# Kernel optimization log

Measured on AMD Instinct MI355X. Metric: run time of the kernel, lower is better.

Reference implementation:

```python
import jax, jax.numpy as jnp
import numpy as np

B, C, H, W = 8, 256, 128, 128
BN_EPS = 1e-5

def setup_inputs() -> dict:
    key = jax.random.key(0)
    ks = jax.random.split(key, 7)
    scale = 1.0 / np.sqrt(C)
    x = jax.random.normal(ks[0], (B, C, H, W), dtype=jnp.float32)
    w_qkv = jax.random.normal(ks[1], (3 * C, C), dtype=jnp.float32) * scale
    w_proj = jax.random.normal(ks[2], (C, C), dtype=jnp.float32) * scale
    gamma = jax.random.uniform(ks[3], (C,), dtype=jnp.float32)
    beta = jax.random.normal(ks[4], (C,), dtype=jnp.float32)
    running_mean = jax.random.normal(ks[5], (C,), dtype=jnp.float32)
    running_var = jax.random.uniform(ks[6], (C,), dtype=jnp.float32) + 0.5
    return {"x": x, "w_qkv": w_qkv, "w_proj": w_proj, "gamma": gamma,
            "beta": beta, "running_mean": running_mean, "running_var": running_var}

def reference(x, w_qkv, w_proj, gamma, beta, running_mean, running_var):
    b, c, h, w = x.shape
    n = h * w
    xf = x.reshape(b, c, n)                       # flatten spatial
    # 1x1 conv == channel matmul: [3c,c] x [b,c,n] -> [b,3c,n]
    qkv = jnp.einsum('oc,bcn->bon', w_qkv, xf)
    q, k, v = jnp.split(qkv, 3, axis=1)           # each [b,c,n]
    k = jax.nn.softmax(k, axis=-1)                # softmax over spatial
    context = jnp.einsum('bcn,bdn->bcd', k, v)    # k @ v^T, [b,c,c]
    out = jnp.einsum('bcd,bcn->bdn', context, q)  # context^T @ q, [b,c,n]
    out = jnp.einsum('oc,bcn->bon', w_proj, out)  # 1x1 proj
    # BatchNorm (inference form with running stats)
    inv = gamma / jnp.sqrt(running_var + BN_EPS)
    out = out * inv[None, :, None] + (beta - running_mean * inv)[None, :, None]
    out = jax.nn.relu(out)
    return out.reshape(b, c, h, w)
```

## Files before the change

kernel.cpp:

```cpp
#include <hip/hip_runtime.h>
#include <stdint.h>

#define B_   8
#define C_   256
#define N_   16384

typedef __attribute__((ext_vector_type(8))) short bf16x8;
typedef __attribute__((ext_vector_type(4))) float f32x4;

__device__ inline float bf2f(unsigned short h) {
    return __uint_as_float(((unsigned)h) << 16);
}
__device__ inline unsigned short f2bf(float f) {
    unsigned u = __float_as_uint(f);
    u += 0x7FFF + ((u >> 16) & 1);
    return (unsigned short)(u >> 16);
}

__device__ inline void gl_lds16(const void* g, void* l) {
    __builtin_amdgcn_global_load_lds(
        reinterpret_cast<const __attribute__((address_space(1))) unsigned int*>(
            reinterpret_cast<uintptr_t>(g)),
        reinterpret_cast<__attribute__((address_space(3))) unsigned int*>(
            reinterpret_cast<uintptr_t>(l)),
        16, 0, 0);
}

__device__ inline f32x4 mfma16(bf16x8 a, bf16x8 b, f32x4 c) {
    return __builtin_amdgcn_mfma_f32_16x16x32_bf16(a, b, c, 0, 0, 0);
}

__global__ __launch_bounds__(256) void k1_transpose(const float* __restrict__ x,
                                                    unsigned short* __restrict__ xT) {
    __shared__ unsigned short tile[64][65];
    const int b = blockIdx.z, c0 = blockIdx.y * 64, n0 = blockIdx.x * 64;
    const float* xb = x + (size_t)b * C_ * N_;
    const int t = threadIdx.x;
    const int tr = t >> 4, tc4 = (t & 15) * 4;
#pragma unroll
    for (int p = 0; p < 4; p++) {
        const int i = p * 16 + tr;
        const float4 v = *(const float4*)(xb + (size_t)(c0 + i) * N_ + n0 + tc4);
        tile[i][tc4 + 0] = f2bf(v.x);
        tile[i][tc4 + 1] = f2bf(v.y);
        tile[i][tc4 + 2] = f2bf(v.z);
        tile[i][tc4 + 3] = f2bf(v.w);
    }
    __syncthreads();
    unsigned short* xTb = xT + (size_t)b * N_ * C_;
#pragma unroll
    for (int p = 0; p < 4; p++) {
        const int jj = p * 16 + tr;
        ushort4 o;
        o.x = tile[tc4 + 0][jj];
        o.y = tile[tc4 + 1][jj];
        o.z = tile[tc4 + 2][jj];
        o.w = tile[tc4 + 3][jj];
        *(ushort4*)(xTb + (size_t)(n0 + jj) * C_ + c0 + tc4) = o;
    }
}

__global__ __launch_bounds__(256) void k1b_setup(const float* __restrict__ wqkv,
                                                 const float* __restrict__ gamma,
                                                 const float* __restrict__ beta,
                                                 const float* __restrict__ rmean,
                                                 const float* __restrict__ rvar,
                                                 unsigned short* __restrict__ wqkv_bf,
                                                 float* __restrict__ inv,
                                                 float* __restrict__ b2) {
    const int t = threadIdx.x;
    if (blockIdx.x < 192) {
        const int base = blockIdx.x * 1024 + t * 4;
        const float4 v = *(const float4*)(wqkv + base);
        ushort4 o;
        o.x = f2bf(v.x); o.y = f2bf(v.y); o.z = f2bf(v.z); o.w = f2bf(v.w);
        *(ushort4*)(wqkv_bf + base) = o;
    } else {
        const float iv = gamma[t] * rsqrtf(rvar[t] + 1e-5f);
        inv[t] = iv;
        b2[t]  = beta[t] - rmean[t] * iv;
    }
}

__global__ __launch_bounds__(256) void k2_kv(const unsigned short* __restrict__ Wkv,
                                             const unsigned short* __restrict__ xT,
                                             unsigned short* __restrict__ kL,
                                             unsigned short* __restrict__ v) {
    __shared__ __align__(16) unsigned short As[128 * 32];
    __shared__ __align__(16) unsigned short Bs[128 * 32];
    const int b  = blockIdx.z;
    const int m0 = blockIdx.y * 128;
    const int n0 = blockIdx.x * 128;
    const int t = threadIdx.x, wave = t >> 6, lane = t & 63;
    const int wm = wave >> 1, wn = wave & 1;

    const unsigned short* xTb = xT + (size_t)b * N_ * C_;

    const int ch1 = wave * 64 + lane, ch2 = ch1 + 256;
    const int r1 = ch1 >> 2, q1 = ch1 & 3;
    const int r2 = ch2 >> 2, q2 = ch2 & 3;
    unsigned short* ldsA1 = As + wave * 512;
    unsigned short* ldsA2 = As + 2048 + wave * 512;
    unsigned short* ldsB1 = Bs + wave * 512;
    unsigned short* ldsB2 = Bs + 2048 + wave * 512;

    f32x4 acc[4][4];
#pragma unroll
    for (int i = 0; i < 4; i++)
#pragma unroll
        for (int j = 0; j < 4; j++)
#pragma unroll
            for (int r = 0; r < 4; r++) acc[i][j][r] = 0.f;

    const int fr = lane & 15;
    const int fk = (lane >> 4) * 8;

    for (int kk = 0; kk < 256; kk += 32) {
        __syncthreads();
        gl_lds16(Wkv + (size_t)(m0 + r1) * 256 + kk + q1 * 8, ldsA1);
        gl_lds16(Wkv + (size_t)(m0 + r2) * 256 + kk + q2 * 8, ldsA2);
        gl_lds16(xTb + (size_t)(n0 + r1) * 256 + kk + q1 * 8, ldsB1);
        gl_lds16(xTb + (size_t)(n0 + r2) * 256 + kk + q2 * 8, ldsB2);
        __syncthreads();
        bf16x8 af[4], bfv[4];
#pragma unroll
        for (int i = 0; i < 4; i++)
            af[i] = *(const bf16x8*)(As + (wm * 64 + i * 16 + fr) * 32 + fk);
#pragma unroll
        for (int j = 0; j < 4; j++)
            bfv[j] = *(const bf16x8*)(Bs + (wn * 64 + j * 16 + fr) * 32 + fk);
#pragma unroll
        for (int i = 0; i < 4; i++)
#pragma unroll
            for (int j = 0; j < 4; j++)
                acc[i][j] = mfma16(af[i], bfv[j], acc[i][j]);
    }

    const int col = lane & 15, rowq = (lane >> 4) * 4;
    unsigned short* outK = kL + (size_t)b * C_ * N_;
    unsigned short* outV = v  + (size_t)b * C_ * N_;
#pragma unroll
    for (int i = 0; i < 4; i++) {
        const int gm = m0 + wm * 64 + i * 16 + rowq;
#pragma unroll
        for (int j = 0; j < 4; j++) {
            const int gn = n0 + wn * 64 + j * 16 + col;
#pragma unroll
            for (int r = 0; r < 4; r++) {
                const int m = gm + r;
                const unsigned short hv = f2bf(acc[i][j][r]);
                if (m < 256) outK[(size_t)m * N_ + gn] = hv;
                else         outV[(size_t)(m - 256) * N_ + gn] = hv;
            }
        }
    }
}

__global__ __launch_bounds__(256) void k3_stats(const unsigned short* __restrict__ kL,
                                                float* __restrict__ rmax,
                                                float* __restrict__ rsum) {
    const size_t rowbase = (size_t)blockIdx.x * N_;
    const int t = threadIdx.x;
    uint4 d[8];
#pragma unroll
    for (int i = 0; i < 8; i++)
        d[i] = *(const uint4*)(kL + rowbase + (size_t)(i * 256 + t) * 8);
    float m = -3.4e38f;
#pragma unroll
    for (int i = 0; i < 8; i++) {
        const unsigned short* p = (const unsigned short*)&d[i];
#pragma unroll
        for (int e = 0; e < 8; e++) m = fmaxf(m, bf2f(p[e]));
    }
#pragma unroll
    for (int o = 1; o < 64; o <<= 1) m = fmaxf(m, __shfl_xor(m, o, 64));
    __shared__ float red[4];
    __shared__ float red2[4];
    if ((t & 63) == 0) red[t >> 6] = m;
    __syncthreads();
    m = fmaxf(fmaxf(red[0], red[1]), fmaxf(red[2], red[3]));
    float s = 0.f;
#pragma unroll
    for (int i = 0; i < 8; i++) {
        const unsigned short* p = (const unsigned short*)&d[i];
#pragma unroll
        for (int e = 0; e < 8; e++) s += __expf(bf2f(p[e]) - m);
    }
#pragma unroll
    for (int o = 1; o < 64; o <<= 1) s += __shfl_xor(s, o, 64);
    if ((t & 63) == 0) red2[t >> 6] = s;
    __syncthreads();
    if (t == 0) {
        rmax[blockIdx.x] = m;
        rsum[blockIdx.x] = red2[0] + red2[1] + red2[2] + red2[3];
    }
}

__global__ __launch_bounds__(256) void k4_ctx(const unsigned short* __restrict__ kL,
                                              const unsigned short* __restrict__ v,
                                              const float* __restrict__ rmax,
                                              float* __restrict__ ctx) {
    __shared__ __align__(16) unsigned short As[128 * 32];
    __shared__ __align__(16) unsigned short Bs[128 * 32];
    const int bz = blockIdx.z;
    const int b = bz >> 3, s = bz & 7;
    const int m0 = blockIdx.y * 128;
    const int n0 = blockIdx.x * 128;
    const int t = threadIdx.x, wave = t >> 6, lane = t & 63;
    const int wm = wave >> 1, wn = wave & 1;

    const unsigned short* kb = kL + (size_t)b * C_ * N_;
    const unsigned short* vb = v  + (size_t)b * C_ * N_;

    const int ch1 = wave * 64 + lane, ch2 = ch1 + 256;
    const int r1 = ch1 >> 2, q1 = ch1 & 3;
    const int r2 = ch2 >> 2, q2 = ch2 & 3;
    const float mx1 = rmax[b * 256 + m0 + r1];
    const float mx2 = rmax[b * 256 + m0 + r2];
    unsigned short* ldsB1 = Bs + wave * 512;
    unsigned short* ldsB2 = Bs + 2048 + wave * 512;

    f32x4 acc[4][4];
#pragma unroll
    for (int i = 0; i < 4; i++)
#pragma unroll
        for (int j = 0; j < 4; j++)
#pragma unroll
            for (int r = 0; r < 4; r++) acc[i][j][r] = 0.f;

    const int fr = lane & 15;
    const int fk = (lane >> 4) * 8;
    const int kbase = s * 2048;

    for (int kk = kbase; kk < kbase + 2048; kk += 32) {
        __syncthreads();
        gl_lds16(vb + (size_t)(n0 + r1) * N_ + kk + q1 * 8, ldsB1);
        gl_lds16(vb + (size_t)(n0 + r2) * N_ + kk + q2 * 8, ldsB2);
        const uint4 a1 = *(const uint4*)(kb + (size_t)(m0 + r1) * N_ + kk + q1 * 8);
        const uint4 a2 = *(const uint4*)(kb + (size_t)(m0 + r2) * N_ + kk + q2 * 8);
        uint4 e1, e2;
        {
            const unsigned short* p = (const unsigned short*)&a1;
            unsigned short* o = (unsigned short*)&e1;
#pragma unroll
            for (int e = 0; e < 8; e++) o[e] = f2bf(__expf(bf2f(p[e]) - mx1));
        }
        {
            const unsigned short* p = (const unsigned short*)&a2;
            unsigned short* o = (unsigned short*)&e2;
#pragma unroll
            for (int e = 0; e < 8; e++) o[e] = f2bf(__expf(bf2f(p[e]) - mx2));
        }
        *(uint4*)(As + r1 * 32 + q1 * 8) = e1;
        *(uint4*)(As + r2 * 32 + q2 * 8) = e2;
        __syncthreads();
        bf16x8 af[4], bfv[4];
#pragma unroll
        for (int i = 0; i < 4; i++)
            af[i] = *(const bf16x8*)(As + (wm * 64 + i * 16 + fr) * 32 + fk);
#pragma unroll
        for (int j = 0; j < 4; j++)
            bfv[j] = *(const bf16x8*)(Bs + (wn * 64 + j * 16 + fr) * 32 + fk);
#pragma unroll
        for (int i = 0; i < 4; i++)
#pragma unroll
            for (int j = 0; j < 4; j++)
                acc[i][j] = mfma16(af[i], bfv[j], acc[i][j]);
    }

    float* cb = ctx + (size_t)b * C_ * C_;
    const int col = lane & 15, rowq = (lane >> 4) * 4;
#pragma unroll
    for (int i = 0; i < 4; i++) {
        const int gc = m0 + wm * 64 + i * 16 + rowq;
#pragma unroll
        for (int j = 0; j < 4; j++) {
            const int gd = n0 + wn * 64 + j * 16 + col;
#pragma unroll
            for (int r = 0; r < 4; r++)
                atomicAdd(&cb[(size_t)(gc + r) * C_ + gd], acc[i][j][r]);
        }
    }
}

__global__ __launch_bounds__(256) void k5a_T(const float* __restrict__ Wp,
                                             const float* __restrict__ ctx,
                                             const float* __restrict__ rsum,
                                             float* __restrict__ T) {
    __shared__ float Asm[64][65];
    __shared__ float Bsm[64][65];
    const int b = blockIdx.z;
    const int o0 = blockIdx.y * 64, c0 = blockIdx.x * 64;
    const int t = threadIdx.x;
    const int tm = t >> 4, tn = t & 15;
    const int lc4 = tn * 4;
    float acc[4][4] = {};
    const float* cb = ctx + (size_t)b * C_ * C_;
    for (int kk = 0; kk < 256; kk += 64) {
        __syncthreads();
#pragma unroll
        for (int p = 0; p < 4; p++) {
            const int r = p * 16 + tm;
            const float4 av = *(const float4*)(Wp + (size_t)(o0 + r) * C_ + kk + lc4);
            Asm[r][lc4] = av.x; Asm[r][lc4 + 1] = av.y; Asm[r][lc4 + 2] = av.z; Asm[r][lc4 + 3] = av.w;
            const float4 bv = *(const float4*)(cb + (size_t)(c0 + r) * C_ + kk + lc4);
            Bsm[r][lc4] = bv.x; Bsm[r][lc4 + 1] = bv.y; Bsm[r][lc4 + 2] = bv.z; Bsm[r][lc4 + 3] = bv.w;
        }
        __syncthreads();
        for (int k = 0; k < 64; k++) {
            float a_[4], b_[4];
#pragma unroll
            for (int i = 0; i < 4; i++) a_[i] = Asm[tm * 4 + i][k];
#pragma unroll
            for (int j = 0; j < 4; j++) b_[j] = Bsm[tn * 4 + j][k];
#pragma unroll
            for (int i = 0; i < 4; i++)
#pragma unroll
                for (int j = 0; j < 4; j++) acc[i][j] += a_[i] * b_[j];
        }
    }
    float isv[4];
#pragma unroll
    for (int j = 0; j < 4; j++) isv[j] = 1.f / rsum[b * 256 + c0 + tn * 4 + j];
#pragma unroll
    for (int i = 0; i < 4; i++)
#pragma unroll
        for (int j = 0; j < 4; j++)
            T[((size_t)b * C_ + o0 + tm * 4 + i) * C_ + c0 + tn * 4 + j] = acc[i][j] * isv[j];
}

__global__ __launch_bounds__(256) void k5b_G(const float* __restrict__ Tm,
                                             const float* __restrict__ Wq,
                                             const float* __restrict__ inv,
                                             unsigned short* __restrict__ G) {
    __shared__ float Asm[64][65];
    __shared__ float Bsm[64][65];
    const int b = blockIdx.z;
    const int o0 = blockIdx.y * 64, j0 = blockIdx.x * 64;
    const int t = threadIdx.x;
    const int tm = t >> 4, tn = t & 15;
    const int lc4 = tn * 4;
    float acc[4][4] = {};
    const float* Tb = Tm + (size_t)b * C_ * C_;
    for (int kk = 0; kk < 256; kk += 64) {
        __syncthreads();
#pragma unroll
        for (int p = 0; p < 4; p++) {
            const int r = p * 16 + tm;
            const float4 av = *(const float4*)(Tb + (size_t)(o0 + r) * C_ + kk + lc4);
            Asm[r][lc4] = av.x; Asm[r][lc4 + 1] = av.y; Asm[r][lc4 + 2] = av.z; Asm[r][lc4 + 3] = av.w;
            const float4 bv = *(const float4*)(Wq + (size_t)(kk + r) * C_ + j0 + lc4);
            Bsm[r][lc4] = bv.x; Bsm[r][lc4 + 1] = bv.y; Bsm[r][lc4 + 2] = bv.z; Bsm[r][lc4 + 3] = bv.w;
        }
        __syncthreads();
        for (int k = 0; k < 64; k++) {
            float a_[4], b_[4];
#pragma unroll
            for (int i = 0; i < 4; i++) a_[i] = Asm[tm * 4 + i][k];
#pragma unroll
            for (int j = 0; j < 4; j++) b_[j] = Bsm[k][tn * 4 + j];
#pragma unroll
            for (int i = 0; i < 4; i++)
#pragma unroll
                for (int j = 0; j < 4; j++) acc[i][j] += a_[i] * b_[j];
        }
    }
#pragma unroll
    for (int i = 0; i < 4; i++) {
        const float iv = inv[o0 + tm * 4 + i];
#pragma unroll
        for (int j = 0; j < 4; j++)
            G[((size_t)b * C_ + o0 + tm * 4 + i) * C_ + j0 + tn * 4 + j] = f2bf(acc[i][j] * iv);
    }
}

__global__ __launch_bounds__(256) void k6_out(const unsigned short* __restrict__ G,
                                              const unsigned short* __restrict__ xT,
                                              const float* __restrict__ b2,
                                              float* __restrict__ out) {
    __shared__ __align__(16) unsigned short As[128 * 32];
    __shared__ __align__(16) unsigned short Bs[128 * 32];
    const int b  = blockIdx.z;
    const int m0 = blockIdx.y * 128;
    const int n0 = blockIdx.x * 128;
    const int t = threadIdx.x, wave = t >> 6, lane = t & 63;
    const int wm = wave >> 1, wn = wave & 1;

    const unsigned short* Gb  = G  + (size_t)b * C_ * C_;
    const unsigned short* xTb = xT + (size_t)b * N_ * C_;

    const int ch1 = wave * 64 + lane, ch2 = ch1 + 256;
    const int r1 = ch1 >> 2, q1 = ch1 & 3;
    const int r2 = ch2 >> 2, q2 = ch2 & 3;
    unsigned short* ldsA1 = As + wave * 512;
    unsigned short* ldsA2 = As + 2048 + wave * 512;
    unsigned short* ldsB1 = Bs + wave * 512;
    unsigned short* ldsB2 = Bs + 2048 + wave * 512;

    f32x4 acc[4][4];
#pragma unroll
    for (int i = 0; i < 4; i++)
#pragma unroll
        for (int j = 0; j < 4; j++)
#pragma unroll
            for (int r = 0; r < 4; r++) acc[i][j][r] = 0.f;

    const int fr = lane & 15;
    const int fk = (lane >> 4) * 8;

    for (int kk = 0; kk < 256; kk += 32) {
        __syncthreads();
        gl_lds16(Gb  + (size_t)(m0 + r1) * 256 + kk + q1 * 8, ldsA1);
        gl_lds16(Gb  + (size_t)(m0 + r2) * 256 + kk + q2 * 8, ldsA2);
        gl_lds16(xTb + (size_t)(n0 + r1) * 256 + kk + q1 * 8, ldsB1);
        gl_lds16(xTb + (size_t)(n0 + r2) * 256 + kk + q2 * 8, ldsB2);
        __syncthreads();
        bf16x8 af[4], bfv[4];
#pragma unroll
        for (int i = 0; i < 4; i++)
            af[i] = *(const bf16x8*)(As + (wm * 64 + i * 16 + fr) * 32 + fk);
#pragma unroll
        for (int j = 0; j < 4; j++)
            bfv[j] = *(const bf16x8*)(Bs + (wn * 64 + j * 16 + fr) * 32 + fk);
#pragma unroll
        for (int i = 0; i < 4; i++)
#pragma unroll
            for (int j = 0; j < 4; j++)
                acc[i][j] = mfma16(af[i], bfv[j], acc[i][j]);
    }

    const int col = lane & 15, rowq = (lane >> 4) * 4;
    float* ob = out + (size_t)b * C_ * N_;
#pragma unroll
    for (int i = 0; i < 4; i++) {
        const int gm = m0 + wm * 64 + i * 16 + rowq;
#pragma unroll
        for (int j = 0; j < 4; j++) {
            const int gn = n0 + wn * 64 + j * 16 + col;
#pragma unroll
            for (int r = 0; r < 4; r++) {
                const float val = fmaxf(acc[i][j][r] + b2[gm + r], 0.f);
                ob[(size_t)(gm + r) * N_ + gn] = val;
            }
        }
    }
}

extern "C" void kernel_launch(void* const* d_in, const int* in_sizes, int n_in,
                              void* d_out, int out_size, void* d_ws, size_t ws_size,
                              hipStream_t stream) {
    const float* x     = (const float*)d_in[0];
    const float* wqkv  = (const float*)d_in[1];
    const float* wproj = (const float*)d_in[2];
    const float* gamma = (const float*)d_in[3];
    const float* beta  = (const float*)d_in[4];
    const float* rmean = (const float*)d_in[5];
    const float* rvar  = (const float*)d_in[6];
    float* out = (float*)d_out;

    char* ws = (char*)d_ws;
    size_t off = 0;
    auto alloc = [&](size_t bytes) {
        void* p = ws + off;
        off += (bytes + 255) & ~(size_t)255;
        return p;
    };
    unsigned short* xT      = (unsigned short*)alloc((size_t)B_ * N_ * C_ * 2);
    unsigned short* kL      = (unsigned short*)alloc((size_t)B_ * C_ * N_ * 2);
    unsigned short* vv      = (unsigned short*)alloc((size_t)B_ * C_ * N_ * 2);
    unsigned short* wqkv_bf = (unsigned short*)alloc((size_t)768 * 256 * 2);
    float* rmax = (float*)alloc(2048 * 4);
    float* rsum = (float*)alloc(2048 * 4);
    float* invp = (float*)alloc(256 * 4);
    float* b2p  = (float*)alloc(256 * 4);
    float* ctx  = (float*)alloc((size_t)B_ * C_ * C_ * 4);
    float* Tm   = (float*)alloc((size_t)B_ * C_ * C_ * 4);
    unsigned short* G = (unsigned short*)alloc((size_t)B_ * C_ * C_ * 2);

    hipLaunchKernelGGL(k1_transpose, dim3(256, 4, 8), dim3(256), 0, stream, x, xT);
    hipLaunchKernelGGL(k1b_setup, dim3(193), dim3(256), 0, stream,
                       wqkv, gamma, beta, rmean, rvar, wqkv_bf, invp, b2p);
    hipLaunchKernelGGL(k2_kv, dim3(128, 4, 8), dim3(256), 0, stream,
                       wqkv_bf + 256 * 256, xT, kL, vv);
    hipLaunchKernelGGL(k3_stats, dim3(2048), dim3(256), 0, stream, kL, rmax, rsum);
    hipMemsetAsync(ctx, 0, (size_t)B_ * C_ * C_ * 4, stream);
    hipLaunchKernelGGL(k4_ctx, dim3(2, 2, 64), dim3(256), 0, stream, kL, vv, rmax, ctx);
    hipLaunchKernelGGL(k5a_T, dim3(4, 4, 8), dim3(256), 0, stream, wproj, ctx, rsum, Tm);
    hipLaunchKernelGGL(k5b_G, dim3(4, 4, 8), dim3(256), 0, stream, Tm, wqkv, invp, G);
    hipLaunchKernelGGL(k6_out, dim3(128, 2, 8), dim3(256), 0, stream, G, xT, b2p, out);
}
```

Baseline: 447.0 us.

## Fuse K/V projection, softmax exponent and context GEMM into one kernel

Replaces the separate K/V projection, softmax-statistics and context kernels with a single kernel. Each block computes K and V tiles for 512 spatial positions from double-buffered, swizzled xT tiles in LDS and exponentiates K in registers. It accumulates row sums, then multiplies exp(K) by V from LDS into a per-block context accumulator that is flushed with atomics. This removes the round trip of the large bf16 K and V intermediates through global memory and two kernel launches. The trade-off is that softmax drops max subtraction, which risks overflow for large logits, and the per-lane W fragments are prepacked and read straight from global/L2.

New measurement: 582.7 us. 30.3% more time.

```diff
diff --git a/kernel.cpp b/kernel.cpp
--- a/kernel.cpp
+++ b/kernel.cpp
@@ -8,9 +8,6 @@
 typedef __attribute__((ext_vector_type(8))) short bf16x8;
 typedef __attribute__((ext_vector_type(4))) float f32x4;
 
-__device__ inline float bf2f(unsigned short h) {
-    return __uint_as_float(((unsigned)h) << 16);
-}
 __device__ inline unsigned short f2bf(float f) {
     unsigned u = __float_as_uint(f);
     u += 0x7FFF + ((u >> 16) & 1);
@@ -65,16 +62,25 @@
                                                  const float* __restrict__ beta,
                                                  const float* __restrict__ rmean,
                                                  const float* __restrict__ rvar,
-                                                 unsigned short* __restrict__ wqkv_bf,
+                                                 unsigned short* __restrict__ WkvF,
                                                  float* __restrict__ inv,
                                                  float* __restrict__ b2) {
     const int t = threadIdx.x;
-    if (blockIdx.x < 192) {
-        const int base = blockIdx.x * 1024 + t * 4;
-        const float4 v = *(const float4*)(wqkv + base);
-        ushort4 o;
-        o.x = f2bf(v.x); o.y = f2bf(v.y); o.z = f2bf(v.z); o.w = f2bf(v.w);
-        *(ushort4*)(wqkv_bf + base) = o;
+    if (blockIdx.x < 64) {
+        const int chunk = blockIdx.x * 256 + t;
+        const int lane = chunk & 63;
+        const int kb = (chunk >> 6) & 7;
+        const int rb = chunk >> 9;
+        const int row = rb * 16 + (lane & 15);
+        const int k0 = kb * 32 + (lane >> 4) * 8;
+        const float* src = wqkv + (size_t)(256 + row) * 256 + k0;
+        const float4 a = *(const float4*)(src);
+        const float4 c = *(const float4*)(src + 4);
+        ushort4 o0, o1;
+        o0.x = f2bf(a.x); o0.y = f2bf(a.y); o0.z = f2bf(a.z); o0.w = f2bf(a.w);
+        o1.x = f2bf(c.x); o1.y = f2bf(c.y); o1.z = f2bf(c.z); o1.w = f2bf(c.w);
+        *(ushort4*)(WkvF + (size_t)chunk * 8) = o0;
+        *(ushort4*)(WkvF + (size_t)chunk * 8 + 4) = o1;
     } else {
         const float iv = gamma[t] * rsqrtf(rvar[t] + 1e-5f);
         inv[t] = iv;
@@ -82,205 +88,146 @@
     }
 }
 
-__global__ __launch_bounds__(256) void k2_kv(const unsigned short* __restrict__ Wkv,
-                                             const unsigned short* __restrict__ xT,
-                                             unsigned short* __restrict__ kL,
-                                             unsigned short* __restrict__ v) {
-    __shared__ __align__(16) unsigned short As[128 * 32];
-    __shared__ __align__(16) unsigned short Bs[128 * 32];
-    const int b  = blockIdx.z;
-    const int m0 = blockIdx.y * 128;
-    const int n0 = blockIdx.x * 128;
+__global__ __launch_bounds__(512, 2) void k2_ctx(const unsigned short* __restrict__ WkvF,
+                                                 const unsigned short* __restrict__ xT,
+                                                 float* __restrict__ ctx,
+                                                 float* __restrict__ rsum) {
+    __shared__ __align__(16) unsigned short xs[2][64 * 256];
+    __shared__ __align__(16) unsigned short kvs[512 * 64];
+    const int b  = blockIdx.y;
+    const int n0 = blockIdx.x * 512;
     const int t = threadIdx.x, wave = t >> 6, lane = t & 63;
-    const int wm = wave >> 1, wn = wave & 1;
-
+    const int fr = lane & 15, fkq = lane >> 4;
+    const int wr = wave >> 1, wc = wave & 1;
     const unsigned short* xTb = xT + (size_t)b * N_ * C_;
 
-    const int ch1 = wave * 64 + lane, ch2 = ch1 + 256;
-    const int r1 = ch1 >> 2, q1 = ch1 & 3;
-    const int r2 = ch2 >> 2, q2 = ch2 & 3;
-    unsigned short* ldsA1 = As + wave * 512;
-    unsigned short* ldsA2 = As + 2048 + wave * 512;
-    unsigned short* ldsB1 = Bs + wave * 512;
-    unsigned short* ldsB2 = Bs + 2048 + wave * 512;
-
-    f32x4 acc[4][4];
+    f32x4 acc[4][8];
 #pragma unroll
     for (int i = 0; i < 4; i++)
 #pragma unroll
-        for (int j = 0; j < 4; j++)
+        for (int j = 0; j < 8; j++)
 #pragma unroll
             for (int r = 0; r < 4; r++) acc[i][j][r] = 0.f;
-
-    const int fr = lane & 15;
-    const int fk = (lane >> 4) * 8;
-
-    for (int kk = 0; kk < 256; kk += 32) {
-        __syncthreads();
-        gl_lds16(Wkv + (size_t)(m0 + r1) * 256 + kk + q1 * 8, ldsA1);
-        gl_lds16(Wkv + (size_t)(m0 + r2) * 256 + kk + q2 * 8, ldsA2);
-        gl_lds16(xTb + (size_t)(n0 + r1) * 256 + kk + q1 * 8, ldsB1);
-        gl_lds16(xTb + (size_t)(n0 + r2) * 256 + kk + q2 * 8, ldsB2);
-        __syncthreads();
-        bf16x8 af[4], bfv[4];
-#pragma unroll
-        for (int i = 0; i < 4; i++)
-            af[i] = *(const bf16x8*)(As + (wm * 64 + i * 16 + fr) * 32 + fk);
-#pragma unroll
-        for (int j = 0; j < 4; j++)
-            bfv[j] = *(const bf16x8*)(Bs + (wn * 64 + j * 16 + fr) * 32 + fk);
-#pragma unroll
-        for (int i = 0; i < 4; i++)
-#pragma unroll
-            for (int j = 0; j < 4; j++)
-                acc[i][j] = mfma16(af[i], bfv[j], acc[i][j]);
-    }
-
-    const int col = lane & 15, rowq = (lane >> 4) * 4;
-    unsigned short* outK = kL + (size_t)b * C_ * N_;
-    unsigned short* outV = v  + (size_t)b * C_ * N_;
+    float rsacc[2][4];
+#pragma unroll
+    for (int i = 0; i < 2; i++)
+#pragma unroll
+        for (int r = 0; r < 4; r++) rsacc[i][r] = 0.f;
+
+    auto stage = [&](int buf, int sc) {
+        const int nb = n0 + sc * 64;
+#pragma unroll
+        for (int it = 0; it < 4; it++) {
+            const int idx = it * 512 + t;
+            const int r = idx >> 5;
+            const int c = (idx & 31) * 8;
+            const int csw = c ^ ((r & 7) * 8);
+            gl_lds16(xTb + (size_t)(nb + r) * 256 + csw,
+                     &xs[buf][it * 4096 + wave * 512]);
+        }
+    };
+
+    stage(0, 0);
+    __syncthreads();
+
+    for (int s = 0; s < 8; ++s) {
+        const int cur = s & 1;
+        if (s < 7) stage(cur ^ 1, s + 1);
+
+#pragma unroll
+        for (int p = 0; p < 2; ++p) {
+            f32x4 kacc[2][4];
+#pragma unroll
+            for (int i = 0; i < 2; i++)
+#pragma unroll
+                for (int j = 0; j < 4; j++)
+#pragma unroll
+                    for (int r = 0; r < 4; r++) kacc[i][j][r] = 0.f;
+#pragma unroll
+            for (int kb = 0; kb < 8; kb++) {
+                bf16x8 bfv[4];
+#pragma unroll
+                for (int j = 0; j < 4; j++) {
+                    const int rr = j * 16 + fr;
+                    const int cs = (kb * 32 + fkq * 8) ^ ((rr & 7) * 8);
+                    bfv[j] = *(const bf16x8*)(&xs[cur][rr * 256 + cs]);
+                }
+#pragma unroll
+                for (int i = 0; i < 2; i++) {
+                    const int rb = p * 16 + 2 * wave + i;
+                    const bf16x8 af = *(const bf16x8*)(
+                        WkvF + (((size_t)rb * 8 + kb) * 64 + lane) * 8);
+#pragma unroll
+                    for (int j = 0; j < 4; j++)
+                        kacc[i][j] = mfma16(af, bfv[j], kacc[i][j]);
+                }
+            }
+#pragma unroll
+            for (int i = 0; i < 2; i++) {
+                const int rowb = p * 256 + 32 * wave + i * 16 + fkq * 4;
+#pragma unroll
+                for (int j = 0; j < 4; j++) {
+                    const int cn = j * 16 + fr;
+#pragma unroll
+                    for (int r = 0; r < 4; r++) {
+                        float vv = kacc[i][j][r];
+                        if (p == 0) { vv = __expf(vv); rsacc[i][r] += vv; }
+                        const int row = rowb + r;
+                        kvs[row * 64 + (cn ^ ((row & 7) * 8))] = f2bf(vv);
+                    }
+                }
+            }
+        }
+        __syncthreads();
+
+#pragma unroll
+        for (int kk = 0; kk < 2; kk++) {
+            bf16x8 a2[4], b2v[8];
+#pragma unroll
+            for (int i = 0; i < 4; i++) {
+                const int row = wr * 64 + i * 16 + fr;
+                const int cs = (kk * 32 + fkq * 8) ^ ((row & 7) * 8);
+                a2[i] = *(const bf16x8*)(&kvs[row * 64 + cs]);
+            }
+#pragma unroll
+            for (int j = 0; j < 8; j++) {
+                const int row = 256 + wc * 128 + j * 16 + fr;
+                const int cs = (kk * 32 + fkq * 8) ^ ((row & 7) * 8);
+                b2v[j] = *(const bf16x8*)(&kvs[row * 64 + cs]);
+            }
+#pragma unroll
+            for (int i = 0; i < 4; i++)
+#pragma unroll
+                for (int j = 0; j < 8; j++)
+                    acc[i][j] = mfma16(a2[i], b2v[j], acc[i][j]);
+        }
+        __syncthreads();
+    }
+
+    float* cb = ctx + (size_t)b * C_ * C_;
 #pragma unroll
     for (int i = 0; i < 4; i++) {
-        const int gm = m0 + wm * 64 + i * 16 + rowq;
-#pragma unroll
-        for (int j = 0; j < 4; j++) {
-            const int gn = n0 + wn * 64 + j * 16 + col;
-#pragma unroll
-            for (int r = 0; r < 4; r++) {
-                const int m = gm + r;
-                const unsigned short hv = f2bf(acc[i][j][r]);
-                if (m < 256) outK[(size_t)m * N_ + gn] = hv;
-                else         outV[(size_t)(m - 256) * N_ + gn] = hv;
-            }
-        }
-    }
-}
-
-__global__ __launch_bounds__(256) void k3_stats(const unsigned short* __restrict__ kL,
-                                                float* __restrict__ rmax,
-                                                float* __restrict__ rsum) {
-    const size_t rowbase = (size_t)blockIdx.x * N_;
-    const int t = threadIdx.x;
-    uint4 d[8];
-#pragma unroll
-    for (int i = 0; i < 8; i++)
-        d[i] = *(const uint4*)(kL + rowbase + (size_t)(i * 256 + t) * 8);
-    float m = -3.4e38f;
-#pragma unroll
-    for (int i = 0; i < 8; i++) {
-        const unsigned short* p = (const unsigned short*)&d[i];
-#pragma unroll
-        for (int e = 0; e < 8; e++) m = fmaxf(m, bf2f(p[e]));
-    }
-#pragma unroll
-    for (int o = 1; o < 64; o <<= 1) m = fmaxf(m, __shfl_xor(m, o, 64));
-    __shared__ float red[4];
-    __shared__ float red2[4];
-    if ((t & 63) == 0) red[t >> 6] = m;
-    __syncthreads();
-    m = fmaxf(fmaxf(red[0], red[1]), fmaxf(red[2], red[3]));
-    float s = 0.f;
-#pragma unroll
-    for (int i = 0; i < 8; i++) {
-        const unsigned short* p = (const unsigned short*)&d[i];
-#pragma unroll
-        for (int e = 0; e < 8; e++) s += __expf(bf2f(p[e]) - m);
-    }
-#pragma unroll
-    for (int o = 1; o < 64; o <<= 1) s += __shfl_xor(s, o, 64);
-    if ((t & 63) == 0) red2[t >> 6] = s;
-    __syncthreads();
-    if (t == 0) {
-        rmax[blockIdx.x] = m;
-        rsum[blockIdx.x] = red2[0] + red2[1] + red2[2] + red2[3];
-    }
-}
-
-__global__ __launch_bounds__(256) void k4_ctx(const unsigned short* __restrict__ kL,
-                                              const unsigned short* __restrict__ v,
-                                              const float* __restrict__ rmax,
-                                              float* __restrict__ ctx) {
-    __shared__ __align__(16) unsigned short As[128 * 32];
-    __shared__ __align__(16) unsigned short Bs[128 * 32];
-    const int bz = blockIdx.z;
-    const int b = bz >> 3, s = bz & 7;
-    const int m0 = blockIdx.y * 128;
-    const int n0 = blockIdx.x * 128;
-    const int t = threadIdx.x, wave = t >> 6, lane = t & 63;
-    const int wm = wave >> 1, wn = wave & 1;
-
-    const unsigned short* kb = kL + (size_t)b * C_ * N_;
-    const unsigned short* vb = v  + (size_t)b * C_ * N_;
-
-    const int ch1 = wave * 64 + lane, ch2 = ch1 + 256;
-    const int r1 = ch1 >> 2, q1 = ch1 & 3;
-    const int r2 = ch2 >> 2, q2 = ch2 & 3;
-    const float mx1 = rmax[b * 256 + m0 + r1];
-    const float mx2 = rmax[b * 256 + m0 + r2];
-    unsigned short* ldsB1 = Bs + wave * 512;
-    unsigned short* ldsB2 = Bs + 2048 + wave * 512;
-
-    f32x4 acc[4][4];
-#pragma unroll
-    for (int i = 0; i < 4; i++)
-#pragma unroll
-        for (int j = 0; j < 4; j++)
-#pragma unroll
-            for (int r = 0; r < 4; r++) acc[i][j][r] = 0.f;
-
-    const int fr = lane & 15;
-    const int fk = (lane >> 4) * 8;
-    const int kbase = s * 2048;
-
-    for (int kk = kbase; kk < kbase + 2048; kk += 32) {
-        __syncthreads();
-        gl_lds16(vb + (size_t)(n0 + r1) * N_ + kk + q1 * 8, ldsB1);
-        gl_lds16(vb + (size_t)(n0 + r2) * N_ + kk + q2 * 8, ldsB2);
-        const uint4 a1 = *(const uint4*)(kb + (size_t)(m0 + r1) * N_ + kk + q1 * 8);
-        const uint4 a2 = *(const uint4*)(kb + (size_t)(m0 + r2) * N_ + kk + q2 * 8);
-        uint4 e1, e2;
-        {
-            const unsigned short* p = (const unsigned short*)&a1;
-            unsigned short* o = (unsigned short*)&e1;
-#pragma unroll
-            for (int e = 0; e < 8; e++) o[e] = f2bf(__expf(bf2f(p[e]) - mx1));
-        }
-        {
-            const unsigned short* p = (const unsigned short*)&a2;
-            unsigned short* o = (unsigned short*)&e2;
-#pragma unroll
-            for (int e = 0; e < 8; e++) o[e] = f2bf(__expf(bf2f(p[e]) - mx2));
-        }
-        *(uint4*)(As + r1 * 32 + q1 * 8) = e1;
-        *(uint4*)(As + r2 * 32 + q2 * 8) = e2;
-        __syncthreads();
-        bf16x8 af[4], bfv[4];
-#pragma unroll
-        for (int i = 0; i < 4; i++)
-            af[i] = *(const bf16x8*)(As + (wm * 64 + i * 16 + fr) * 32 + fk);
-#pragma unroll
-        for (int j = 0; j < 4; j++)
-            bfv[j] = *(const bf16x8*)(Bs + (wn * 64 + j * 16 + fr) * 32 + fk);
-#pragma unroll
-        for (int i = 0; i < 4; i++)
-#pragma unroll
-            for (int j = 0; j < 4; j++)
-                acc[i][j] = mfma16(af[i], bfv[j], acc[i][j]);
-    }
-
-    float* cb = ctx + (size_t)b * C_ * C_;
-    const int col = lane & 15, rowq = (lane >> 4) * 4;
-#pragma unroll
-    for (int i = 0; i < 4; i++) {
-        const int gc = m0 + wm * 64 + i * 16 + rowq;
-#pragma unroll
-        for (int j = 0; j < 4; j++) {
-            const int gd = n0 + wn * 64 + j * 16 + col;
+        const int gc = wr * 64 + i * 16 + fkq * 4;
+#pragma unroll
+        for (int j = 0; j < 8; j++) {
+            const int gd = wc * 128 + j * 16 + fr;
 #pragma unroll
             for (int r = 0; r < 4; r++)
                 atomicAdd(&cb[(size_t)(gc + r) * C_ + gd], acc[i][j][r]);
         }
     }
+#pragma unroll
+    for (int i = 0; i < 2; i++)
+#pragma unroll
+        for (int r = 0; r < 4; r++) {
+            float sv = rsacc[i][r];
+            sv += __shfl_xor(sv, 1, 64);
+            sv += __shfl_xor(sv, 2, 64);
+            sv += __shfl_xor(sv, 4, 64);
+            sv += __shfl_xor(sv, 8, 64);
+            if (fr == 0)
+                atomicAdd(&rsum[b * 256 + 32 * wave + i * 16 + fkq * 4 + r], sv);
+        }
 }
 
 __global__ __launch_bounds__(256) void k5a_T(const float* __restrict__ Wp,
@@ -465,26 +412,20 @@
         off += (bytes + 255) & ~(size_t)255;
         return p;
     };
-    unsigned short* xT      = (unsigned short*)alloc((size_t)B_ * N_ * C_ * 2);
-    unsigned short* kL      = (unsigned short*)alloc((size_t)B_ * C_ * N_ * 2);
-    unsigned short* vv      = (unsigned short*)alloc((size_t)B_ * C_ * N_ * 2);
-    unsigned short* wqkv_bf = (unsigned short*)alloc((size_t)768 * 256 * 2);
-    float* rmax = (float*)alloc(2048 * 4);
-    float* rsum = (float*)alloc(2048 * 4);
+    unsigned short* xT   = (unsigned short*)alloc((size_t)B_ * N_ * C_ * 2);
+    unsigned short* WkvF = (unsigned short*)alloc((size_t)512 * 256 * 2);
     float* invp = (float*)alloc(256 * 4);
     float* b2p  = (float*)alloc(256 * 4);
     float* ctx  = (float*)alloc((size_t)B_ * C_ * C_ * 4);
+    float* rsum = (float*)alloc(2048 * 4);
     float* Tm   = (float*)alloc((size_t)B_ * C_ * C_ * 4);
     unsigned short* G = (unsigned short*)alloc((size_t)B_ * C_ * C_ * 2);
 
     hipLaunchKernelGGL(k1_transpose, dim3(256, 4, 8), dim3(256), 0, stream, x, xT);
-    hipLaunchKernelGGL(k1b_setup, dim3(193), dim3(256), 0, stream,
-                       wqkv, gamma, beta, rmean, rvar, wqkv_bf, invp, b2p);
-    hipLaunchKernelGGL(k2_kv, dim3(128, 4, 8), dim3(256), 0, stream,
-                       wqkv_bf + 256 * 256, xT, kL, vv);
-    hipLaunchKernelGGL(k3_stats, dim3(2048), dim3(256), 0, stream, kL, rmax, rsum);
-    hipMemsetAsync(ctx, 0, (size_t)B_ * C_ * C_ * 4, stream);
-    hipLaunchKernelGGL(k4_ctx, dim3(2, 2, 64), dim3(256), 0, stream, kL, vv, rmax, ctx);
+    hipLaunchKernelGGL(k1b_setup, dim3(65), dim3(256), 0, stream,
+                       wqkv, gamma, beta, rmean, rvar, WkvF, invp, b2p);
+    hipMemsetAsync(ctx, 0, (size_t)B_ * C_ * C_ * 4 + 2048 * 4, stream);
+    hipLaunchKernelGGL(k2_ctx, dim3(32, 8), dim3(512), 0, stream, WkvF, xT, ctx, rsum);
     hipLaunchKernelGGL(k5a_T, dim3(4, 4, 8), dim3(256), 0, stream, wproj, ctx, rsum, Tm);
     hipLaunchKernelGGL(k5b_G, dim3(4, 4, 8), dim3(256), 0, stream, Tm, wqkv, invp, G);
     hipLaunchKernelGGL(k6_out, dim3(128, 2, 8), dim3(256), 0, stream, G, xT, b2p, out);
```
